# Kernel tuning notes

Hardware: AMD Instinct MI355X
Metric: run time of the kernel (lower is better)

The kernel has to match this reference:

```python
import jax, jax.numpy as jnp
import numpy as np

K = 24            # patch_size (window)
D = 4             # dilation
C = 256           # dim
H = 8             # num_heads
N = 500000        # number of octree tokens at this depth (nnum_t)
BATCH_SIZE = 8
BLOCK = K * D
NA = int(np.ceil(N / BLOCK)) * BLOCK   # nnum_a (padded length)
PAD = NA - N
SCALE = (C // H) ** -0.5
MASK_VAL = -1000.0


def setup_inputs() -> dict:
    key = jax.random.key(0)
    k1, k2, k3, k4 = jax.random.split(key, 4)
    data = jax.random.normal(k1, (N, C), jnp.float32)
    qkv_w = jax.random.normal(k2, (3 * C, C), jnp.float32) * 0.02
    qkv_b = jnp.zeros((3 * C,), jnp.float32)
    proj_w = jax.random.normal(k3, (C, C), jnp.float32) * 0.02
    proj_b = jnp.zeros((C,), jnp.float32)
    batch_idx = jnp.sort(jax.random.randint(k4, (N,), 0, BATCH_SIZE, dtype=jnp.int32))
    return {"data": data, "qkv_w": qkv_w, "qkv_b": qkv_b,
            "proj_w": proj_w, "proj_b": proj_b, "batch_idx": batch_idx}


def _dilate_mask(batch_idx):
    # patch_partition of batch ids: pad with fill_value = batch_size
    b = jnp.concatenate([batch_idx, jnp.full((PAD,), BATCH_SIZE, jnp.int32)], axis=0)
    # dilate reshuffle: (-1, K, D) -> transpose -> (-1, K) windows
    b = b.reshape(-1, K, D).transpose(0, 2, 1).reshape(-1, K)
    diff = b[:, :, None] - b[:, None, :]           # [nw, K, K]
    return jnp.where(diff != 0, MASK_VAL, 0.0).astype(jnp.float32)


def reference(data, qkv_w, qkv_b, proj_w, proj_b, batch_idx):
    mask = _dilate_mask(batch_idx)                              # [nw, K, K]
    # patch_partition of features: pad with zeros
    x = jnp.concatenate([data, jnp.zeros((PAD, C), data.dtype)], axis=0)
    # dilation reshuffle: (-1, K, D, C) -> (-1, D, K, C) -> windows [nw, K, C]
    x = x.reshape(-1, K, D, C).transpose(0, 2, 1, 3).reshape(-1, K, C)
    qkv = (x @ qkv_w.T + qkv_b).reshape(-1, K, 3, H, C // H).transpose(2, 0, 3, 1, 4)
    q, k, v = qkv[0] * SCALE, qkv[1], qkv[2]                    # [nw, H, K, hd]
    attn = jnp.einsum('nhqd,nhkd->nhqk', q, k) + mask[:, None]  # [nw, H, K, K]
    attn = jax.nn.softmax(attn, axis=-1)
    out = jnp.einsum('nhqk,nhkd->nhqd', attn, v)
    out = out.transpose(0, 2, 1, 3).reshape(-1, C)              # merge heads
    # reverse dilation reshuffle, drop padding (patch_reverse)
    out = out.reshape(-1, D, K, C).transpose(0, 2, 1, 3).reshape(-1, C)[:N]
    return out @ proj_w.T + proj_b
```

## Files before the change

### kernel.cpp

```cpp
#include <hip/hip_runtime.h>


#define N_TOK 500000
#define NA    500064
#define MP    500096
#define CDIM  256
#define KWIN  24
#define NWIN  20836
#define HEADS 8
#define HDIM  32
#define SCALE_F 0.17677669529663689f
#define MASKV  -1000.0f

typedef __attribute__((ext_vector_type(8))) short bf16x8;
typedef __attribute__((ext_vector_type(4))) float f32x4;

__device__ __forceinline__ unsigned short f2b(float f) {
    unsigned int u = __float_as_uint(f);
    u += 0x7fffu + ((u >> 16) & 1u);
    return (unsigned short)(u >> 16);
}
__device__ __forceinline__ float b2f_lo(unsigned int x) { return __uint_as_float(x << 16); }
__device__ __forceinline__ float b2f_hi(unsigned int x) { return __uint_as_float(x & 0xffff0000u); }

#define GLOAD_LDS16(gsrc, ldst) \
    __builtin_amdgcn_global_load_lds((const __attribute__((address_space(1))) void*)(gsrc), \
                                     (__attribute__((address_space(3))) void*)(ldst), 16, 0, 0)


__global__ __launch_bounds__(256) void cvt_data_kernel(const float* __restrict__ src,
                                                       unsigned short* __restrict__ dst) {
    long long i = (long long)blockIdx.x * 256 + threadIdx.x;
    long long base = i * 8;
    int row = (int)(base >> 8);
    uint4 o;
    if (row < N_TOK) {
        float4 a = *(const float4*)(src + base);
        float4 b = *(const float4*)(src + base + 4);
        o.x = (unsigned)f2b(a.x) | ((unsigned)f2b(a.y) << 16);
        o.y = (unsigned)f2b(a.z) | ((unsigned)f2b(a.w) << 16);
        o.z = (unsigned)f2b(b.x) | ((unsigned)f2b(b.y) << 16);
        o.w = (unsigned)f2b(b.z) | ((unsigned)f2b(b.w) << 16);
    } else {
        o = make_uint4(0u, 0u, 0u, 0u);
    }
    *(uint4*)(dst + base) = o;
}

__global__ __launch_bounds__(256) void cvt_w_kernel(const float* __restrict__ src,
                                                    unsigned short* __restrict__ dst, int n8) {
    int i = blockIdx.x * 256 + threadIdx.x;
    if (i >= n8) return;
    float4 a = ((const float4*)src)[i * 2];
    float4 b = ((const float4*)src)[i * 2 + 1];
    uint4 o;
    o.x = (unsigned)f2b(a.x) | ((unsigned)f2b(a.y) << 16);
    o.y = (unsigned)f2b(a.z) | ((unsigned)f2b(a.w) << 16);
    o.z = (unsigned)f2b(b.x) | ((unsigned)f2b(b.y) << 16);
    o.w = (unsigned)f2b(b.z) | ((unsigned)f2b(b.w) << 16);
    ((uint4*)dst)[i] = o;
}

__global__ __launch_bounds__(256) void zero_pad_kernel(unsigned short* __restrict__ dst) {
    int i = blockIdx.x * 256 + threadIdx.x;
    if (i < (MP - N_TOK) * CDIM / 8)
        *(uint4*)(dst + (size_t)N_TOK * CDIM + (size_t)i * 8) = make_uint4(0u, 0u, 0u, 0u);
}


template<int NN, bool OUT_F32>
__global__ __launch_bounds__(256, 2) void gemm_kernel(const unsigned short* __restrict__ A,
                                                      const unsigned short* __restrict__ Bt,
                                                      const float* __restrict__ bias,
                                                      void* __restrict__ out_p,
                                                      int m_write) {
    __shared__ unsigned short ldsA[128 * 64];
    __shared__ unsigned short ldsB[128 * 64];
    const int tid  = threadIdx.x;
    const int lane = tid & 63;
    const int wv   = tid >> 6;
    const int wr   = wv >> 1, wc = wv & 1;
    const int mtile = blockIdx.y, ntile = blockIdx.x;

    f32x4 acc[4][4];
    #pragma unroll
    for (int i = 0; i < 4; ++i) {
        #pragma unroll
        for (int j = 0; j < 4; ++j) {
            #pragma unroll
            for (int r = 0; r < 4; ++r) acc[i][j][r] = 0.f;
        }
    }

    const char* abase = (const char*)(A  + (size_t)mtile * 128 * CDIM);
    const char* bbase = (const char*)(Bt + (size_t)ntile * 128 * CDIM);
    const int lrow8 = lane >> 3;
    const int lcolb = (lane & 7) * 16;

    for (int kt = 0; kt < 4; ++kt) {
        const int kb_byte = kt * 128;
        #pragma unroll
        for (int c = 0; c < 4; ++c) {
            int chunk = wv * 4 + c;
            int row = chunk * 8 + lrow8;
            GLOAD_LDS16(abase + (size_t)row * 512 + kb_byte + lcolb, &ldsA[chunk * 512]);
        }
        #pragma unroll
        for (int c = 0; c < 4; ++c) {
            int chunk = wv * 4 + c;
            int row = chunk * 8 + lrow8;
            GLOAD_LDS16(bbase + (size_t)row * 512 + kb_byte + lcolb, &ldsB[chunk * 512]);
        }
        __syncthreads();
        #pragma unroll
        for (int ks = 0; ks < 2; ++ks) {
            const int kb = ks * 32 + (lane >> 4) * 8;
            bf16x8 af[4], bfr[4];
            #pragma unroll
            for (int i = 0; i < 4; ++i) {
                af[i]  = *(const bf16x8*)&ldsA[(wr * 64 + i * 16 + (lane & 15)) * 64 + kb];
                bfr[i] = *(const bf16x8*)&ldsB[(wc * 64 + i * 16 + (lane & 15)) * 64 + kb];
            }
            #pragma unroll
            for (int i = 0; i < 4; ++i) {
                #pragma unroll
                for (int j = 0; j < 4; ++j)
                    acc[i][j] = __builtin_amdgcn_mfma_f32_16x16x32_bf16(af[i], bfr[j], acc[i][j], 0, 0, 0);
            }
        }
        __syncthreads();
    }

    #pragma unroll
    for (int i = 0; i < 4; ++i) {
        int row0 = mtile * 128 + wr * 64 + i * 16 + ((lane >> 4) << 2);
        #pragma unroll
        for (int j = 0; j < 4; ++j) {
            int col = ntile * 128 + wc * 64 + j * 16 + (lane & 15);
            float bv = bias[col];
            #pragma unroll
            for (int r = 0; r < 4; ++r) {
                int row = row0 + r;
                float v = acc[i][j][r] + bv;
                if (OUT_F32) {
                    if (row < m_write) ((float*)out_p)[(size_t)row * NN + col] = v;
                } else {
                    ((unsigned short*)out_p)[(size_t)row * NN + col] = f2b(v);
                }
            }
        }
    }
}


__global__ __launch_bounds__(256) void attn_kernel(const unsigned short* __restrict__ qkv,
                                                   const int* __restrict__ batch_idx,
                                                   unsigned short* __restrict__ attn_out) {
    __shared__ unsigned short sq[KWIN * 768];
    __shared__ int sbi[KWIN];
    const int w = blockIdx.x;
    const int g = w >> 2, dd = w & 3;
    const int tid = threadIdx.x;
    const int wv = tid >> 6;

    #pragma unroll
    for (int c = 0; c < 9; ++c) {
        int chunk = c * 256 + tid;
        int row = chunk / 96;
        int within = chunk - row * 96;
        int p = g * 96 + row * 4 + dd;
        const char* src = (const char*)qkv + (size_t)p * 1536 + within * 16;
        GLOAD_LDS16(src, &sq[(c * 256 + wv * 64) * 8]);
    }
    if (tid < KWIN) {
        int p = g * 96 + tid * 4 + dd;
        sbi[tid] = (p < N_TOK) ? batch_idx[p] : 8;
    }
    __syncthreads();

    const int h = tid / 24;
    const int q = tid - h * 24;
    if (h < HEADS) {
        float Q[32];
        const unsigned int* qp = (const unsigned int*)&sq[q * 768 + h * 32];
        #pragma unroll
        for (int c = 0; c < 16; ++c) {
            unsigned int x = qp[c];
            Q[c * 2]     = b2f_lo(x);
            Q[c * 2 + 1] = b2f_hi(x);
        }
        const int bq = sbi[q];
        float s[KWIN];
        float mx = -3.0e38f;
        for (int k = 0; k < KWIN; ++k) {
            const unsigned int* kp = (const unsigned int*)&sq[k * 768 + 256 + h * 32];
            float dot = 0.f;
            #pragma unroll
            for (int c = 0; c < 16; ++c) {
                unsigned int x = kp[c];
                dot += Q[c * 2] * b2f_lo(x) + Q[c * 2 + 1] * b2f_hi(x);
            }
            float v = dot * SCALE_F + ((sbi[k] == bq) ? 0.f : MASKV);
            s[k] = v;
            mx = fmaxf(mx, v);
        }
        float sum = 0.f;
        for (int k = 0; k < KWIN; ++k) { float e = __expf(s[k] - mx); s[k] = e; sum += e; }
        const float inv = 1.f / sum;
        float O[32];
        #pragma unroll
        for (int c = 0; c < 32; ++c) O[c] = 0.f;
        for (int k = 0; k < KWIN; ++k) {
            float pw = s[k] * inv;
            const unsigned int* vp = (const unsigned int*)&sq[k * 768 + 512 + h * 32];
            #pragma unroll
            for (int c = 0; c < 16; ++c) {
                unsigned int x = vp[c];
                O[c * 2]     += pw * b2f_lo(x);
                O[c * 2 + 1] += pw * b2f_hi(x);
            }
        }
        int p = g * 96 + q * 4 + dd;
        if (p < N_TOK) {
            uint4* op = (uint4*)(attn_out + (size_t)p * CDIM + h * HDIM);
            #pragma unroll
            for (int c = 0; c < 4; ++c) {
                uint4 o;
                o.x = (unsigned)f2b(O[c * 8 + 0]) | ((unsigned)f2b(O[c * 8 + 1]) << 16);
                o.y = (unsigned)f2b(O[c * 8 + 2]) | ((unsigned)f2b(O[c * 8 + 3]) << 16);
                o.z = (unsigned)f2b(O[c * 8 + 4]) | ((unsigned)f2b(O[c * 8 + 5]) << 16);
                o.w = (unsigned)f2b(O[c * 8 + 6]) | ((unsigned)f2b(O[c * 8 + 7]) << 16);
                op[c] = o;
            }
        }
    }
}


extern "C" void kernel_launch(void* const* d_in, const int* in_sizes, int n_in,
                              void* d_out, int out_size, void* d_ws, size_t ws_size,
                              hipStream_t stream) {
    const float* data    = (const float*)d_in[0];
    const float* qkv_w   = (const float*)d_in[1];
    const float* qkv_b   = (const float*)d_in[2];
    const float* proj_w  = (const float*)d_in[3];
    const float* proj_b  = (const float*)d_in[4];
    const int*   batch_i = (const int*)d_in[5];

    char* ws = (char*)d_ws;
    size_t off = 0;
    unsigned short* dataB  = (unsigned short*)(ws + off); off += (size_t)MP * CDIM * 2;
    unsigned short* qkvB   = (unsigned short*)(ws + off); off += (size_t)MP * 768 * 2;
    unsigned short* attnB  = (unsigned short*)(ws + off); off += (size_t)MP * CDIM * 2;
    unsigned short* wqkvB  = (unsigned short*)(ws + off); off += (size_t)768 * 256 * 2;
    unsigned short* wprojB = (unsigned short*)(ws + off); off += (size_t)256 * 256 * 2;
    if (ws_size < off) return;

    cvt_data_kernel<<<MP / 8, 256, 0, stream>>>(data, dataB);
    cvt_w_kernel<<<(768 * 256 / 8 + 255) / 256, 256, 0, stream>>>(qkv_w, wqkvB, 768 * 256 / 8);
    cvt_w_kernel<<<(256 * 256 / 8 + 255) / 256, 256, 0, stream>>>(proj_w, wprojB, 256 * 256 / 8);
    zero_pad_kernel<<<12, 256, 0, stream>>>(attnB);

    gemm_kernel<768, false><<<dim3(6, MP / 128), 256, 0, stream>>>(dataB, wqkvB, qkv_b, qkvB, MP);
    attn_kernel<<<NWIN, 256, 0, stream>>>(qkvB, batch_i, attnB);
    gemm_kernel<256, true><<<dim3(2, MP / 128), 256, 0, stream>>>(attnB, wprojB, proj_b, d_out, N_TOK);
}
```

Baseline: 1.092 ms.

## Rewrite window attention to use MFMA per (window, head) wavefront

Replaces the scalar per-thread attention (one thread per query/head with LDS-staged QKV) with one wavefront per (window, head) that loads Q/K fragments directly from global memory and computes QK^T and PV with 16x16x32 bf16 MFMA. Softmax is done in registers with cross-lane shuffles, and probabilities are staged through swizzled LDS to form the A operand. This removes the large LDS staging and the scalar FMA work. In exchange it pads the 24-token window to 32, uses scattered scalar V loads and 2-byte output stores, and quantizes the probabilities to bf16.

```diff
diff --git a/kernel.cpp b/kernel.cpp
--- a/kernel.cpp
+++ b/kernel.cpp
@@ -8,9 +8,7 @@
 #define KWIN  24
 #define NWIN  20836
 #define HEADS 8
-#define HDIM  32
 #define SCALE_F 0.17677669529663689f
-#define MASKV  -1000.0f
 
 typedef __attribute__((ext_vector_type(8))) short bf16x8;
 typedef __attribute__((ext_vector_type(4))) float f32x4;
@@ -20,8 +18,6 @@
     u += 0x7fffu + ((u >> 16) & 1u);
     return (unsigned short)(u >> 16);
 }
-__device__ __forceinline__ float b2f_lo(unsigned int x) { return __uint_as_float(x << 16); }
-__device__ __forceinline__ float b2f_hi(unsigned int x) { return __uint_as_float(x & 0xffff0000u); }
 
 #define GLOAD_LDS16(gsrc, ldst) \
     __builtin_amdgcn_global_load_lds((const __attribute__((address_space(1))) void*)(gsrc), \
@@ -156,84 +152,138 @@
 __global__ __launch_bounds__(256) void attn_kernel(const unsigned short* __restrict__ qkv,
                                                    const int* __restrict__ batch_idx,
                                                    unsigned short* __restrict__ attn_out) {
-    __shared__ unsigned short sq[KWIN * 768];
-    __shared__ int sbi[KWIN];
-    const int w = blockIdx.x;
-    const int g = w >> 2, dd = w & 3;
-    const int tid = threadIdx.x;
-    const int wv = tid >> 6;
-
-    #pragma unroll
-    for (int c = 0; c < 9; ++c) {
-        int chunk = c * 256 + tid;
-        int row = chunk / 96;
-        int within = chunk - row * 96;
-        int p = g * 96 + row * 4 + dd;
-        const char* src = (const char*)qkv + (size_t)p * 1536 + within * 16;
-        GLOAD_LDS16(src, &sq[(c * 256 + wv * 64) * 8]);
-    }
-    if (tid < KWIN) {
-        int p = g * 96 + tid * 4 + dd;
-        sbi[tid] = (p < N_TOK) ? batch_idx[p] : 8;
-    }
-    __syncthreads();
-
-    const int h = tid / 24;
-    const int q = tid - h * 24;
-    if (h < HEADS) {
-        float Q[32];
-        const unsigned int* qp = (const unsigned int*)&sq[q * 768 + h * 32];
-        #pragma unroll
-        for (int c = 0; c < 16; ++c) {
-            unsigned int x = qp[c];
-            Q[c * 2]     = b2f_lo(x);
-            Q[c * 2 + 1] = b2f_hi(x);
-        }
-        const int bq = sbi[q];
-        float s[KWIN];
-        float mx = -3.0e38f;
-        for (int k = 0; k < KWIN; ++k) {
-            const unsigned int* kp = (const unsigned int*)&sq[k * 768 + 256 + h * 32];
-            float dot = 0.f;
-            #pragma unroll
-            for (int c = 0; c < 16; ++c) {
-                unsigned int x = kp[c];
-                dot += Q[c * 2] * b2f_lo(x) + Q[c * 2 + 1] * b2f_hi(x);
-            }
-            float v = dot * SCALE_F + ((sbi[k] == bq) ? 0.f : MASKV);
-            s[k] = v;
-            mx = fmaxf(mx, v);
-        }
-        float sum = 0.f;
-        for (int k = 0; k < KWIN; ++k) { float e = __expf(s[k] - mx); s[k] = e; sum += e; }
-        const float inv = 1.f / sum;
-        float O[32];
-        #pragma unroll
-        for (int c = 0; c < 32; ++c) O[c] = 0.f;
-        for (int k = 0; k < KWIN; ++k) {
-            float pw = s[k] * inv;
-            const unsigned int* vp = (const unsigned int*)&sq[k * 768 + 512 + h * 32];
-            #pragma unroll
-            for (int c = 0; c < 16; ++c) {
-                unsigned int x = vp[c];
-                O[c * 2]     += pw * b2f_lo(x);
-                O[c * 2 + 1] += pw * b2f_hi(x);
-            }
-        }
-        int p = g * 96 + q * 4 + dd;
-        if (p < N_TOK) {
-            uint4* op = (uint4*)(attn_out + (size_t)p * CDIM + h * HDIM);
-            #pragma unroll
-            for (int c = 0; c < 4; ++c) {
-                uint4 o;
-                o.x = (unsigned)f2b(O[c * 8 + 0]) | ((unsigned)f2b(O[c * 8 + 1]) << 16);
-                o.y = (unsigned)f2b(O[c * 8 + 2]) | ((unsigned)f2b(O[c * 8 + 3]) << 16);
-                o.z = (unsigned)f2b(O[c * 8 + 4]) | ((unsigned)f2b(O[c * 8 + 5]) << 16);
-                o.w = (unsigned)f2b(O[c * 8 + 6]) | ((unsigned)f2b(O[c * 8 + 7]) << 16);
-                op[c] = o;
-            }
-        }
-    }
+    __shared__ unsigned short sP[4][32 * 64];
+    const int tid  = threadIdx.x;
+    const int lane = tid & 63;
+    const int ws_  = tid >> 6;
+    const int wid  = blockIdx.x * 4 + ws_;
+    const int w = wid >> 3, h = wid & 7;
+    const int gw = w >> 2, dd = w & 3;
+    const int lrow = lane & 15, lg = lane >> 4;
+    const int pbase = gw * 96 + dd;
+
+    bf16x8 Qf[2], Kf[2];
+    #pragma unroll
+    for (int t = 0; t < 2; ++t) {
+        size_t p = (size_t)(pbase + (t * 16 + lrow) * 4);
+        const unsigned short* bp = qkv + p * 768 + h * 32 + lg * 8;
+        Qf[t] = *(const bf16x8*)bp;
+        Kf[t] = *(const bf16x8*)(bp + 256);
+    }
+
+    unsigned short v0[8], v1[8];
+    #pragma unroll
+    for (int j2 = 0; j2 < 8; ++j2) {
+        size_t p = (size_t)(pbase + (lg * 8 + j2) * 4);
+        const unsigned short* vp = qkv + p * 768 + 512 + h * 32 + lrow;
+        v0[j2] = vp[0];
+        v1[j2] = vp[16];
+    }
+
+    int bq[2];
+    #pragma unroll
+    for (int j = 0; j < 2; ++j) {
+        int r = j * 16 + lrow;
+        int p = pbase + r * 4;
+        bq[j] = (r < KWIN && p < N_TOK) ? batch_idx[p] : -1;
+    }
+    int bk[2][4];
+    #pragma unroll
+    for (int i = 0; i < 2; ++i)
+        #pragma unroll
+        for (int rr = 0; rr < 4; ++rr) {
+            int r = i * 16 + lg * 4 + rr;
+            int p = pbase + r * 4;
+            bk[i][rr] = (r < KWIN && p < N_TOK) ? batch_idx[p] : -2;
+        }
+
+    f32x4 accS[2][2];
+    #pragma unroll
+    for (int i = 0; i < 2; ++i)
+        #pragma unroll
+        for (int j = 0; j < 2; ++j)
+            #pragma unroll
+            for (int r = 0; r < 4; ++r) accS[i][j][r] = 0.f;
+    #pragma unroll
+    for (int i = 0; i < 2; ++i)
+        #pragma unroll
+        for (int j = 0; j < 2; ++j)
+            accS[i][j] = __builtin_amdgcn_mfma_f32_16x16x32_bf16(Kf[i], Qf[j], accS[i][j], 0, 0, 0);
+
+    float sv[2][2][4];
+    float mx[2] = { -3.0e38f, -3.0e38f };
+    #pragma unroll
+    for (int i = 0; i < 2; ++i)
+        #pragma unroll
+        for (int j = 0; j < 2; ++j)
+            #pragma unroll
+            for (int rr = 0; rr < 4; ++rr) {
+                float val = (bk[i][rr] == bq[j]) ? accS[i][j][rr] * SCALE_F : -1.0e9f;
+                sv[i][j][rr] = val;
+                mx[j] = fmaxf(mx[j], val);
+            }
+    mx[0] = fmaxf(mx[0], __shfl_xor(mx[0], 16)); mx[0] = fmaxf(mx[0], __shfl_xor(mx[0], 32));
+    mx[1] = fmaxf(mx[1], __shfl_xor(mx[1], 16)); mx[1] = fmaxf(mx[1], __shfl_xor(mx[1], 32));
+    float sm[2] = { 0.f, 0.f };
+    #pragma unroll
+    for (int i = 0; i < 2; ++i)
+        #pragma unroll
+        for (int j = 0; j < 2; ++j)
+            #pragma unroll
+            for (int rr = 0; rr < 4; ++rr) {
+                float e = __expf(sv[i][j][rr] - mx[j]);
+                sv[i][j][rr] = e;
+                sm[j] += e;
+            }
+    sm[0] += __shfl_xor(sm[0], 16); sm[0] += __shfl_xor(sm[0], 32);
+    sm[1] += __shfl_xor(sm[1], 16); sm[1] += __shfl_xor(sm[1], 32);
+    float inv[2] = { 1.f / sm[0], 1.f / sm[1] };
+
+    char* pb = (char*)sP[ws_];
+    const int swz = (lrow & 7) << 4;
+    #pragma unroll
+    for (int j = 0; j < 2; ++j) {
+        int q = j * 16 + lrow;
+        #pragma unroll
+        for (int i = 0; i < 2; ++i) {
+            unsigned lo = (unsigned)f2b(sv[i][j][0] * inv[j]) | ((unsigned)f2b(sv[i][j][1] * inv[j]) << 16);
+            unsigned hi = (unsigned)f2b(sv[i][j][2] * inv[j]) | ((unsigned)f2b(sv[i][j][3] * inv[j]) << 16);
+            *(uint2*)(pb + q * 128 + ((i * 32 + lg * 8) ^ swz)) = make_uint2(lo, hi);
+        }
+    }
+    bf16x8 AP[2];
+    #pragma unroll
+    for (int jj = 0; jj < 2; ++jj)
+        AP[jj] = *(const bf16x8*)(pb + (jj * 16 + lrow) * 128 + ((lg * 16) ^ swz));
+
+    union { bf16x8 v; unsigned short s[8]; } B0, B1;
+    #pragma unroll
+    for (int j2 = 0; j2 < 8; ++j2) { B0.s[j2] = v0[j2]; B1.s[j2] = v1[j2]; }
+    f32x4 accO[2][2];
+    #pragma unroll
+    for (int i = 0; i < 2; ++i)
+        #pragma unroll
+        for (int j = 0; j < 2; ++j)
+            #pragma unroll
+            for (int r = 0; r < 4; ++r) accO[i][j][r] = 0.f;
+    #pragma unroll
+    for (int jj = 0; jj < 2; ++jj) {
+        accO[jj][0] = __builtin_amdgcn_mfma_f32_16x16x32_bf16(AP[jj], B0.v, accO[jj][0], 0, 0, 0);
+        accO[jj][1] = __builtin_amdgcn_mfma_f32_16x16x32_bf16(AP[jj], B1.v, accO[jj][1], 0, 0, 0);
+    }
+
+    #pragma unroll
+    for (int jj = 0; jj < 2; ++jj)
+        #pragma unroll
+        for (int rr = 0; rr < 4; ++rr) {
+            int q = jj * 16 + lg * 4 + rr;
+            int p = pbase + q * 4;
+            if (q < KWIN && p < N_TOK) {
+                unsigned short* op = attn_out + (size_t)p * CDIM + h * 32;
+                op[lrow]      = f2b(accO[jj][0][rr]);
+                op[16 + lrow] = f2b(accO[jj][1][rr]);
+            }
+        }
 }
 
 
@@ -262,6 +312,6 @@
     zero_pad_kernel<<<12, 256, 0, stream>>>(attnB);
 
     gemm_kernel<768, false><<<dim3(6, MP / 128), 256, 0, stream>>>(dataB, wqkvB, qkv_b, qkvB, MP);
-    attn_kernel<<<NWIN, 256, 0, stream>>>(qkvB, batch_i, attnB);
+    attn_kernel<<<NWIN * HEADS / 4, 256, 0, stream>>>(qkvB, batch_i, attnB);
     gemm_kernel<256, true><<<dim3(2, MP / 128), 256, 0, stream>>>(attnB, wprojB, proj_b, d_out, N_TOK);
 }
```

New measurement: 1.007 ms. 1.08x faster.
